# Optimization experiments

Measured on AMD Instinct MI355X. Metric: run time of the kernel, lower is better.

Reference implementation:

```python
import jax, jax.numpy as jnp
import numpy as np

# dims
B, T = 256, 64
N_AG, N_FEAT = 10, 4
X_DIM, X_PERM, X_STATIC = 44, 40, 10
HID, XEMB, NHID = 128, 32, 8
E = N_AG * (N_AG - 1)           # 90 directed edges (off-diagonal)
GEMB = NHID * E                 # 720 graph embedding per sample/step
RNN_IN = XEMB + 1 + GEMB        # 753
A_IN = X_STATIC + GEMB          # 730 (x_emb_size2==0 in GraphNN branch)
O_IN = XEMB + X_STATIC + 1 + GEMB  # 763

_off = np.ones((N_AG, N_AG)) - np.eye(N_AG)
RECV = jnp.asarray(np.where(_off)[0])  # rel_rec one-hot == gather by receiver idx
SEND = jnp.asarray(np.where(_off)[1])  # rel_send one-hot == gather by sender idx


def setup_inputs() -> dict:
    key = jax.random.key(0)
    ks = jax.random.split(key, 32)
    w = lambda k, shape: jax.random.normal(k, shape, jnp.float32) * 0.05
    return {
        'x': jax.random.normal(ks[0], (B, T + 1, X_DIM), jnp.float32),
        'x_demo': jax.random.normal(ks[1], (B, X_STATIC), jnp.float32),
        'f_treatment': jax.random.uniform(ks[2], (B, T + 1, 1), jnp.float32),
        'h0': jax.random.normal(ks[3], (B, HID), jnp.float32),
        # x2emb (Linear 4->32), x_static2emb (Linear 10->10)
        'W_x2emb': w(ks[4], (XEMB, X_DIM - X_PERM)), 'b_x2emb': w(ks[5], (XEMB,)),
        'W_stat': w(ks[6], (X_STATIC, X_STATIC)), 'b_stat': w(ks[7], (X_STATIC,)),
        # NRI-style MLP1 (node): 4->8->8 ; MLP2 (edge): 16->8->8
        'W_m1a': w(ks[8], (NHID, N_FEAT)), 'b_m1a': w(ks[9], (NHID,)),
        'W_m1b': w(ks[10], (NHID, NHID)), 'b_m1b': w(ks[11], (NHID,)),
        'W_m2a': w(ks[12], (NHID, 2 * NHID)), 'b_m2a': w(ks[13], (NHID,)),
        'W_m2b': w(ks[14], (NHID, NHID)), 'b_m2b': w(ks[15], (NHID,)),
        # treatment head: Linear(730->128)+ReLU, then Linear(128->1, no bias)
        'W_a1': w(ks[16], (HID, A_IN)), 'b_a1': w(ks[17], (HID,)),
        'W_a2': w(ks[18], (1, HID)),
        # outcome head: Linear(763->128)+ReLU, then Linear(128->1, no bias)
        'W_o1': w(ks[19], (HID, O_IN)), 'b_o1': w(ks[20], (HID,)),
        'W_o2': w(ks[21], (1, HID)),
        # GRUCell(753 -> 128)
        'W_ih': w(ks[22], (3 * HID, RNN_IN)), 'b_ih': w(ks[23], (3 * HID,)),
        'W_hh': w(ks[24], (3 * HID, HID)), 'b_hh': w(ks[25], (3 * HID,)),
    }


def reference(x, x_demo, f_treatment, h0, W_x2emb, b_x2emb, W_stat, b_stat,
              W_m1a, b_m1a, W_m1b, b_m1b, W_m2a, b_m2a, W_m2b, b_m2b,
              W_a1, b_a1, W_a2, W_o1, b_o1, W_o2, W_ih, b_ih, W_hh, b_hh):
    xt = x[:, :T]                       # (B,T,44); len_time = x.size(1)-1
    treat = f_treatment[:, :T]          # (B,T,1)
    demo = x_demo @ W_stat.T + b_stat   # (B,10) static embedding
    demoT = jnp.broadcast_to(demo[:, None], (B, T, X_STATIC))

    # --- GNN(x_permuted): mlp1 per node, node2edge gather, mlp2 per edge ---
    xa = xt[..., :X_PERM].reshape(B, T, N_AG, N_FEAT)
    h1 = jax.nn.elu(xa @ W_m1a.T + b_m1a)
    h1 = jax.nn.elu(h1 @ W_m1b.T + b_m1b)         # (B,T,N_AG,8); BN in eval = identity
    edges = jnp.concatenate([h1[:, :, RECV], h1[:, :, SEND]], axis=-1)  # (B,T,E,16)
    h2 = jax.nn.elu(edges @ W_m2a.T + b_m2a)
    h2 = jax.nn.elu(h2 @ W_m2b.T + b_m2b)         # (B,T,E,8)
    gemb = h2.reshape(B, T, GEMB)                 # (B,T,720)

    xemb = xt[..., X_PERM:] @ W_x2emb.T + b_x2emb  # (B,T,32)

    # --- treatment (a_or_ipw) head; dropout identity in eval ---
    a_in = jnp.concatenate([demoT, gemb], axis=-1)          # (B,T,730)
    a_out = jax.nn.relu(a_in @ W_a1.T + b_a1) @ W_a2.T      # (B,T,1)

    # --- outcome head ---
    o_in = jnp.concatenate([xemb, demoT, treat, gemb], axis=-1)  # (B,T,763)
    y_out = jax.nn.relu(o_in @ W_o1.T + b_o1) @ W_o2.T           # (B,T,1)

    # --- GRUCell recurrence over time ---
    rnn_in = jnp.concatenate([xemb, treat, gemb], axis=-1)  # (B,T,753)
    gi = rnn_in @ W_ih.T + b_ih                             # precompute input proj (B,T,3H)

    def step(h, g):
        gh = h @ W_hh.T + b_hh
        i_r, i_z, i_n = jnp.split(g, 3, axis=-1)
        h_r, h_z, h_n = jnp.split(gh, 3, axis=-1)
        r = jax.nn.sigmoid(i_r + h_r)
        z = jax.nn.sigmoid(i_z + h_z)
        n = jnp.tanh(i_n + r * h_n)
        h_new = (1.0 - z) * n + z * h
        return h_new, h_new

    _, hs = jax.lax.scan(step, h0, jnp.swapaxes(gi, 0, 1))
    hs = jnp.swapaxes(hs, 0, 1)                             # (B,T,128)

    return jnp.concatenate([a_out, y_out, hs], axis=-1)     # (B,T,130)
```

## Files before the change

kernel.cpp:

```cpp
#include <hip/hip_runtime.h>
#include <hip/hip_bf16.h>
#include <math.h>

#define BB     256
#define TT     64
#define BT     (BB*TT)
#define XD     44
#define XP     40
#define XS     10
#define HID    128
#define XEMB   32
#define NHID   8
#define NAG    10
#define NEDGE  90
#define GEMB   720
#define KF     768
#define NTOT   640


typedef __bf16  bf16_t;
typedef __bf16  bf16x8 __attribute__((ext_vector_type(8)));
typedef float   floatx4 __attribute__((ext_vector_type(4)));
typedef _Float16 half2_t __attribute__((ext_vector_type(2)));
typedef _Float16 half4_t __attribute__((ext_vector_type(4)));
typedef _Float16 half8_t __attribute__((ext_vector_type(8)));

__device__ __forceinline__ float rcp_fast(float x) { return __builtin_amdgcn_rcpf(x); }
__device__ __forceinline__ float sigmoid_fast(float v) { return rcp_fast(1.f + __expf(-v)); }
__device__ __forceinline__ float tanh_fast(float x) { return 1.f - 2.f * rcp_fast(1.f + __expf(2.f * x)); }
__device__ __forceinline__ float elu_fast(float v) { return v > 0.f ? v : __expf(v) - 1.f; }
__device__ __forceinline__ float fdot2f(half2_t a, half2_t b, float acc) {
  return __builtin_amdgcn_fdot2(a, b, acc, false);
}
__device__ __forceinline__ float dot8h(half8_t a, half8_t b, float acc) {
  acc = fdot2f(half2_t{a[0], a[1]}, half2_t{b[0], b[1]}, acc);
  acc = fdot2f(half2_t{a[2], a[3]}, half2_t{b[2], b[3]}, acc);
  acc = fdot2f(half2_t{a[4], a[5]}, half2_t{b[4], b[5]}, acc);
  acc = fdot2f(half2_t{a[6], a[7]}, half2_t{b[6], b[7]}, acc);
  return acc;
}
__device__ __forceinline__ void lds_barrier() {
  asm volatile("s_waitcnt lgkmcnt(0)" ::: "memory");
  __builtin_amdgcn_s_barrier();
}

__global__ __launch_bounds__(256) void prep_kernel(
    const float* __restrict__ Wa1, const float* __restrict__ ba1,
    const float* __restrict__ Wo1, const float* __restrict__ bo1,
    const float* __restrict__ Wih, const float* __restrict__ bih,
    bf16_t* __restrict__ WT, float* __restrict__ bcat) {
  int idx = blockIdx.x * 256 + threadIdx.x;
  if (idx >= NTOT * KF) return;
  int n = idx / KF, k = idx - n * KF;
  float v = 0.f;
  if (n < 128) {
    if (k >= 32 && k < 42)  v = Wa1[n * 730 + (k - 32)];
    else if (k >= 48)       v = Wa1[n * 730 + 10 + (k - 48)];
  } else if (n < 256) {
    int m = n - 128;
    if (k < 43)             v = Wo1[m * 763 + k];
    else if (k >= 48)       v = Wo1[m * 763 + 43 + (k - 48)];
  } else {
    int m = n - 256;
    if (k < 32)             v = Wih[m * 753 + k];
    else if (k == 42)       v = Wih[m * 753 + 32];
    else if (k >= 48)       v = Wih[m * 753 + 33 + (k - 48)];
  }
  WT[n * KF + k] = (bf16_t)v;
  if (k == 0) {
    bcat[n] = (n < 128) ? ba1[n] : (n < 256 ? bo1[n - 128] : bih[n - 256]);
  }
}

__global__ __launch_bounds__(64) void encoder_kernel(
    const float* __restrict__ x, const float* __restrict__ x_demo,
    const float* __restrict__ ftreat,
    const float* __restrict__ Wm1a, const float* __restrict__ bm1a,
    const float* __restrict__ Wm1b, const float* __restrict__ bm1b,
    const float* __restrict__ Wm2a, const float* __restrict__ bm2a,
    const float* __restrict__ Wm2b, const float* __restrict__ bm2b,
    const float* __restrict__ Wx2e, const float* __restrict__ bx2e,
    const float* __restrict__ Wst, const float* __restrict__ bst,
    bf16_t* __restrict__ F) {
  int blk = blockIdx.x;
  int b = blk >> 4, tc = blk & 15;
  int lane = threadIdx.x;

  __shared__ __align__(16) _Float16 h1sp[NAG * 8];
  __shared__ __align__(16) _Float16 w2aR[64];
  __shared__ __align__(16) _Float16 w2aS[64];
  __shared__ __align__(16) _Float16 w2bp[64];
  __shared__ float demoL[XS];

  if (lane < 8) {
    float4 v0 = *(const float4*)(Wm2a + lane * 16);
    float4 v1 = *(const float4*)(Wm2a + lane * 16 + 4);
    float4 v2 = *(const float4*)(Wm2a + lane * 16 + 8);
    float4 v3 = *(const float4*)(Wm2a + lane * 16 + 12);
    *(half8_t*)&w2aR[lane * 8] = half8_t{
        (_Float16)v0.x, (_Float16)v0.y, (_Float16)v0.z, (_Float16)v0.w,
        (_Float16)v1.x, (_Float16)v1.y, (_Float16)v1.z, (_Float16)v1.w};
    *(half8_t*)&w2aS[lane * 8] = half8_t{
        (_Float16)v2.x, (_Float16)v2.y, (_Float16)v2.z, (_Float16)v2.w,
        (_Float16)v3.x, (_Float16)v3.y, (_Float16)v3.z, (_Float16)v3.w};
    float4 u0 = *(const float4*)(Wm2b + lane * 8);
    float4 u1 = *(const float4*)(Wm2b + lane * 8 + 4);
    *(half8_t*)&w2bp[lane * 8] = half8_t{
        (_Float16)u0.x, (_Float16)u0.y, (_Float16)u0.z, (_Float16)u0.w,
        (_Float16)u1.x, (_Float16)u1.y, (_Float16)u1.z, (_Float16)u1.w};
  }
  if (lane < 10) {
    float s = bst[lane];
#pragma unroll
    for (int j = 0; j < 10; j++) s += x_demo[b * XS + j] * Wst[lane * 10 + j];
    demoL[lane] = s;
  }

  half4_t wA[8]; float bA[8];
  half8_t wB1[8]; float bB1[8];
  float bR[8], bG[8];
#pragma unroll
  for (int o = 0; o < 8; o++) {
    float4 v = *(const float4*)(Wm1a + o * 4);
    wA[o] = half4_t{(_Float16)v.x, (_Float16)v.y, (_Float16)v.z, (_Float16)v.w};
    bA[o] = bm1a[o];
    float4 w0 = *(const float4*)(Wm1b + o * 8);
    float4 w1 = *(const float4*)(Wm1b + o * 8 + 4);
    wB1[o] = half8_t{(_Float16)w0.x, (_Float16)w0.y, (_Float16)w0.z, (_Float16)w0.w,
                     (_Float16)w1.x, (_Float16)w1.y, (_Float16)w1.z, (_Float16)w1.w};
    bB1[o] = bm1b[o];
    bR[o] = bm2a[o];
    bG[o] = bm2b[o];
  }
  half4_t wX; float bX;
  {
    float4 v = *(const float4*)(Wx2e + (lane & 31) * 4);
    wX = half4_t{(_Float16)v.x, (_Float16)v.y, (_Float16)v.z, (_Float16)v.w};
    bX = bx2e[lane & 31];
  }
  __syncthreads();
  float demov = (lane >= 32 && lane < 42) ? demoL[lane - 32] : 0.f;

  for (int ti = 0; ti < 4; ti++) {
    int t = tc * 4 + ti;
    int tok = b * TT + t;
    const float* row = x + (size_t)(b * 65 + t) * XD;
    bf16_t* Frow = F + (size_t)tok * KF;

    if (lane < NAG) {
      float4 xa = *(const float4*)(row + lane * 4);
      half2_t x0{(_Float16)xa.x, (_Float16)xa.y};
      half2_t x1{(_Float16)xa.z, (_Float16)xa.w};
      float h1v[8];
#pragma unroll
      for (int o = 0; o < 8; o++) {
        float s = bA[o];
        s = fdot2f(x0, half2_t{wA[o][0], wA[o][1]}, s);
        s = fdot2f(x1, half2_t{wA[o][2], wA[o][3]}, s);
        h1v[o] = elu_fast(s);
      }
      half2_t e0{(_Float16)h1v[0], (_Float16)h1v[1]};
      half2_t e1{(_Float16)h1v[2], (_Float16)h1v[3]};
      half2_t e2{(_Float16)h1v[4], (_Float16)h1v[5]};
      half2_t e3{(_Float16)h1v[6], (_Float16)h1v[7]};
      half8_t hout;
#pragma unroll
      for (int o = 0; o < 8; o++) {
        float s = bB1[o];
        s = fdot2f(e0, half2_t{wB1[o][0], wB1[o][1]}, s);
        s = fdot2f(e1, half2_t{wB1[o][2], wB1[o][3]}, s);
        s = fdot2f(e2, half2_t{wB1[o][4], wB1[o][5]}, s);
        s = fdot2f(e3, half2_t{wB1[o][6], wB1[o][7]}, s);
        hout[o] = (_Float16)elu_fast(s);
      }
      *(half8_t*)&h1sp[lane * 8] = hout;
    }
    __syncthreads();

#pragma unroll
    for (int q = 0; q < 2; q++) {
      int e = lane + 64 * q;
      if (e < NEDGE) {
        int r = (e * 57) >> 9;
        int sd = e - 9 * r;
        sd += (sd >= r) ? 1 : 0;
        half8_t hr = *(const half8_t*)&h1sp[r * 8];
        half8_t hs = *(const half8_t*)&h1sp[sd * 8];
        float av[8];
#pragma unroll
        for (int o = 0; o < 8; o++) {
          half8_t wr8 = *(const half8_t*)&w2aR[o * 8];
          half8_t ws8 = *(const half8_t*)&w2aS[o * 8];
          float s = bR[o];
          s = dot8h(hr, wr8, s);
          s = dot8h(hs, ws8, s);
          av[o] = elu_fast(s);
        }
        half2_t a0{(_Float16)av[0], (_Float16)av[1]};
        half2_t a1{(_Float16)av[2], (_Float16)av[3]};
        half2_t a2{(_Float16)av[4], (_Float16)av[5]};
        half2_t a3{(_Float16)av[6], (_Float16)av[7]};
        union { bf16_t h[8]; uint4 u; } pk;
#pragma unroll
        for (int o = 0; o < 8; o++) {
          half8_t wb8 = *(const half8_t*)&w2bp[o * 8];
          float s = bG[o];
          s = fdot2f(a0, half2_t{wb8[0], wb8[1]}, s);
          s = fdot2f(a1, half2_t{wb8[2], wb8[3]}, s);
          s = fdot2f(a2, half2_t{wb8[4], wb8[5]}, s);
          s = fdot2f(a3, half2_t{wb8[6], wb8[7]}, s);
          pk.h[o] = (bf16_t)elu_fast(s);
        }
        *(uint4*)(Frow + 48 + e * 8) = pk.u;
      }
    }

    float4 xe = *(const float4*)(row + XP);
    if (lane < 32) {
      float s = bX;
      s = fdot2f(half2_t{(_Float16)xe.x, (_Float16)xe.y}, half2_t{wX[0], wX[1]}, s);
      s = fdot2f(half2_t{(_Float16)xe.z, (_Float16)xe.w}, half2_t{wX[2], wX[3]}, s);
      Frow[lane] = (bf16_t)s;
    } else if (lane < 42) {
      Frow[lane] = (bf16_t)demov;
    } else if (lane == 42) {
      Frow[42] = (bf16_t)ftreat[b * 65 + t];
    } else if (lane < 48) {
      Frow[lane] = (bf16_t)0.f;
    }
    __syncthreads();
  }
}

__global__ __launch_bounds__(256) void gemm_kernel(
    const bf16_t* __restrict__ F, const bf16_t* __restrict__ WT,
    const float* __restrict__ bcat, float* __restrict__ G) {
  __shared__ __align__(16) bf16_t As[128 * 32];
  __shared__ __align__(16) bf16_t Bs[128 * 32];

  int tid  = threadIdx.x;
  int lane = tid & 63;
  int wv   = tid >> 6;
  int wr   = wv >> 1, wc = wv & 1;
  int m0 = blockIdx.x * 128, n0 = blockIdx.y * 128;

  floatx4 acc[4][4];
#pragma unroll
  for (int i = 0; i < 4; i++)
#pragma unroll
    for (int j = 0; j < 4; j++) acc[i][j] = floatx4{0.f, 0.f, 0.f, 0.f};

  int c0 = tid, c1 = tid + 256;
  int r0 = c0 >> 2, p0 = c0 & 3;
  int r1 = c1 >> 2, p1 = c1 & 3;
  int qr = lane >> 4;
  int lr = lane & 15;

  for (int k0 = 0; k0 < KF; k0 += 32) {
    uint4 a0 = *(const uint4*)(F  + (size_t)(m0 + r0) * KF + k0 + p0 * 8);
    uint4 a1 = *(const uint4*)(F  + (size_t)(m0 + r1) * KF + k0 + p1 * 8);
    uint4 b0 = *(const uint4*)(WT + (size_t)(n0 + r0) * KF + k0 + p0 * 8);
    uint4 b1 = *(const uint4*)(WT + (size_t)(n0 + r1) * KF + k0 + p1 * 8);
    __syncthreads();
    ((uint4*)As)[c0] = a0; ((uint4*)As)[c1] = a1;
    ((uint4*)Bs)[c0] = b0; ((uint4*)Bs)[c1] = b1;
    __syncthreads();

    bf16x8 af[4], bf[4];
#pragma unroll
    for (int i = 0; i < 4; i++) {
      af[i] = *(const bf16x8*)(As + (wr * 64 + i * 16 + lr) * 32 + qr * 8);
      bf[i] = *(const bf16x8*)(Bs + (wc * 64 + i * 16 + lr) * 32 + qr * 8);
    }
#pragma unroll
    for (int i = 0; i < 4; i++)
#pragma unroll
      for (int j = 0; j < 4; j++)
        acc[i][j] = __builtin_amdgcn_mfma_f32_16x16x32_bf16(af[i], bf[j], acc[i][j], 0, 0, 0);
  }

#pragma unroll
  for (int i = 0; i < 4; i++) {
#pragma unroll
    for (int j = 0; j < 4; j++) {
      int col = n0 + wc * 64 + j * 16 + lr;
      float bv = bcat[col];
#pragma unroll
      for (int r = 0; r < 4; r++) {
        int row = m0 + wr * 64 + i * 16 + qr * 4 + r;
        G[(size_t)row * NTOT + col] = acc[i][j][r] + bv;
      }
    }
  }
}

__global__ __launch_bounds__(256) void head_kernel(
    const float* __restrict__ G, const float* __restrict__ Wa2,
    const float* __restrict__ Wo2, float* __restrict__ out) {
  int wid  = (blockIdx.x * 256 + threadIdx.x) >> 6;
  int lane = threadIdx.x & 63;
  const float* g = G + (size_t)wid * NTOT;
  float sa = fmaxf(g[lane], 0.f) * Wa2[lane] + fmaxf(g[lane + 64], 0.f) * Wa2[lane + 64];
  float sy = fmaxf(g[128 + lane], 0.f) * Wo2[lane] + fmaxf(g[192 + lane], 0.f) * Wo2[lane + 64];
#pragma unroll
  for (int off = 32; off > 0; off >>= 1) {
    sa += __shfl_down(sa, off, 64);
    sy += __shfl_down(sy, off, 64);
  }
  if (lane == 0) {
    out[(size_t)wid * 130 + 0] = sa;
    out[(size_t)wid * 130 + 1] = sy;
  }
}

__global__ __launch_bounds__(128, 1) void gru_kernel(
    const float* __restrict__ G, const float* __restrict__ h0,
    const float* __restrict__ Whh, const float* __restrict__ bhh,
    float* __restrict__ out) {
  int b = blockIdx.x;
  int tid = threadIdx.x;
  int lane = tid & 63;

  __shared__ unsigned int h2[2][HID / 2];

  const float* gbase = G + (size_t)b * TT * NTOT;

  half2_t wr[64], wz[64], wn[64];
#pragma unroll
  for (int l = 0; l < 64; l++) {
    float2 a = *(const float2*)(Whh + (size_t)tid * HID + 2 * l);
    wr[l] = half2_t{(_Float16)a.x, (_Float16)a.y};
  }
#pragma unroll
  for (int l = 0; l < 64; l++) {
    float2 a = *(const float2*)(Whh + (size_t)(HID + tid) * HID + 2 * l);
    wz[l] = half2_t{(_Float16)a.x, (_Float16)a.y};
  }
#pragma unroll
  for (int l = 0; l < 64; l++) {
    float2 a = *(const float2*)(Whh + (size_t)(2 * HID + tid) * HID + 2 * l);
    wn[l] = half2_t{(_Float16)a.x, (_Float16)a.y};
  }
  float br = bhh[tid], bz = bhh[HID + tid], bn = bhh[2 * HID + tid];

  float hprev = h0[(size_t)b * HID + tid];
  ((_Float16*)h2[0])[tid] = (_Float16)hprev;
  float ir = gbase[256 + tid], iz = gbase[384 + tid], inn = gbase[512 + tid];
  __syncthreads();

  for (int t = 0; t < TT; t++) {
    unsigned int hl = h2[t & 1][lane];
    float nir = 0.f, niz = 0.f, ninn = 0.f;
    if (t + 1 < TT) {
      const float* gn = gbase + (size_t)(t + 1) * NTOT;
      nir  = gn[256 + tid];
      niz  = gn[384 + tid];
      ninn = gn[512 + tid];
    }
    float sr0 = 0.f, sr1 = 0.f, sz0 = 0.f, sz1 = 0.f, sn0 = 0.f, sn1 = 0.f;
#pragma unroll
    for (int l = 0; l < 64; l += 2) {
      int p0 = __builtin_amdgcn_readlane((int)hl, l);
      int p1 = __builtin_amdgcn_readlane((int)hl, l + 1);
      half2_t q0 = __builtin_bit_cast(half2_t, p0);
      half2_t q1 = __builtin_bit_cast(half2_t, p1);
      sr0 = __builtin_amdgcn_fdot2(wr[l],     q0, sr0, false);
      sr1 = __builtin_amdgcn_fdot2(wr[l + 1], q1, sr1, false);
      sz0 = __builtin_amdgcn_fdot2(wz[l],     q0, sz0, false);
      sz1 = __builtin_amdgcn_fdot2(wz[l + 1], q1, sz1, false);
      sn0 = __builtin_amdgcn_fdot2(wn[l],     q0, sn0, false);
      sn1 = __builtin_amdgcn_fdot2(wn[l + 1], q1, sn1, false);
    }
    float r  = sigmoid_fast(ir + sr0 + sr1 + br);
    float z  = sigmoid_fast(iz + sz0 + sz1 + bz);
    float nn = tanh_fast(inn + r * (sn0 + sn1 + bn));
    float hn = (1.f - z) * nn + z * hprev;
    hprev = hn;
    ((_Float16*)h2[(t + 1) & 1])[tid] = (_Float16)hn;
    lds_barrier();
    out[(size_t)(b * TT + t) * 130 + 2 + tid] = hn;
    ir = nir; iz = niz; inn = ninn;
  }
}

extern "C" void kernel_launch(void* const* d_in, const int* in_sizes, int n_in,
                              void* d_out, int out_size, void* d_ws, size_t ws_size,
                              hipStream_t stream) {
  const float* x      = (const float*)d_in[0];
  const float* x_demo = (const float*)d_in[1];
  const float* ftr    = (const float*)d_in[2];
  const float* h0     = (const float*)d_in[3];
  const float* Wx2e   = (const float*)d_in[4];
  const float* bx2e   = (const float*)d_in[5];
  const float* Wst    = (const float*)d_in[6];
  const float* bst    = (const float*)d_in[7];
  const float* Wm1a   = (const float*)d_in[8];
  const float* bm1a   = (const float*)d_in[9];
  const float* Wm1b   = (const float*)d_in[10];
  const float* bm1b   = (const float*)d_in[11];
  const float* Wm2a   = (const float*)d_in[12];
  const float* bm2a   = (const float*)d_in[13];
  const float* Wm2b   = (const float*)d_in[14];
  const float* bm2b   = (const float*)d_in[15];
  const float* Wa1    = (const float*)d_in[16];
  const float* ba1    = (const float*)d_in[17];
  const float* Wa2    = (const float*)d_in[18];
  const float* Wo1    = (const float*)d_in[19];
  const float* bo1    = (const float*)d_in[20];
  const float* Wo2    = (const float*)d_in[21];
  const float* Wih    = (const float*)d_in[22];
  const float* bih    = (const float*)d_in[23];
  const float* Whh    = (const float*)d_in[24];
  const float* bhh    = (const float*)d_in[25];
  float* out = (float*)d_out;

  char* ws = (char*)d_ws;
  bf16_t* F   = (bf16_t*)(ws);
  bf16_t* WT  = (bf16_t*)(ws + 25165824);
  float*  bc  = (float*)(ws + 25165824 + 983040);
  float*  G   = (float*)(ws + 25165824 + 983040 + 2560);

  prep_kernel<<<dim3((NTOT * KF + 255) / 256), dim3(256), 0, stream>>>(
      Wa1, ba1, Wo1, bo1, Wih, bih, WT, bc);
  encoder_kernel<<<dim3(BB * 16), dim3(64), 0, stream>>>(
      x, x_demo, ftr, Wm1a, bm1a, Wm1b, bm1b, Wm2a, bm2a, Wm2b, bm2b,
      Wx2e, bx2e, Wst, bst, F);
  gemm_kernel<<<dim3(BT / 128, NTOT / 128), dim3(256), 0, stream>>>(F, WT, bc, G);
  head_kernel<<<dim3(BT / 4), dim3(256), 0, stream>>>(G, Wa2, Wo2, out);
  gru_kernel<<<dim3(BB), dim3(128), 0, stream>>>(G, h0, Whh, bhh, out);
}
```

Baseline: 228.5 us.

## Batch GRU recurrence over 16 samples per block using bf16 MFMA

The GRU kernel changes from one block per sample, which did dot products with fdot2 and readlane broadcasts of fp16 hidden state, to one block per 16 samples. Each step's h·W_hh product now runs on 16x16x32 bf16 MFMA instructions, with the weight fragments held in registers and the hidden state transposed through double-buffered LDS. The aim is to cut the per-step latency of the serial 64-step recurrence. The trade-offs are that only 16 blocks occupy the GPU and the hidden state is rounded to bf16 instead of fp16, which may reduce accuracy.

```diff
diff --git a/kernel.cpp b/kernel.cpp
--- a/kernel.cpp
+++ b/kernel.cpp
@@ -19,6 +19,7 @@
 
 
 typedef __bf16  bf16_t;
+typedef __bf16  bf16x4 __attribute__((ext_vector_type(4)));
 typedef __bf16  bf16x8 __attribute__((ext_vector_type(8)));
 typedef float   floatx4 __attribute__((ext_vector_type(4)));
 typedef _Float16 half2_t __attribute__((ext_vector_type(2)));
@@ -313,73 +314,117 @@
   }
 }
 
-__global__ __launch_bounds__(128, 1) void gru_kernel(
+__global__ __launch_bounds__(256, 1) void gru_kernel(
     const float* __restrict__ G, const float* __restrict__ h0,
     const float* __restrict__ Whh, const float* __restrict__ bhh,
     float* __restrict__ out) {
-  int b = blockIdx.x;
-  int tid = threadIdx.x;
+  int tid  = threadIdx.x;
+  int w    = tid >> 6;
   int lane = tid & 63;
-
-  __shared__ unsigned int h2[2][HID / 2];
-
-  const float* gbase = G + (size_t)b * TT * NTOT;
-
-  half2_t wr[64], wz[64], wn[64];
-#pragma unroll
-  for (int l = 0; l < 64; l++) {
-    float2 a = *(const float2*)(Whh + (size_t)tid * HID + 2 * l);
-    wr[l] = half2_t{(_Float16)a.x, (_Float16)a.y};
-  }
-#pragma unroll
-  for (int l = 0; l < 64; l++) {
-    float2 a = *(const float2*)(Whh + (size_t)(HID + tid) * HID + 2 * l);
-    wz[l] = half2_t{(_Float16)a.x, (_Float16)a.y};
-  }
-#pragma unroll
-  for (int l = 0; l < 64; l++) {
-    float2 a = *(const float2*)(Whh + (size_t)(2 * HID + tid) * HID + 2 * l);
-    wn[l] = half2_t{(_Float16)a.x, (_Float16)a.y};
-  }
-  float br = bhh[tid], bz = bhh[HID + tid], bn = bhh[2 * HID + tid];
-
-  float hprev = h0[(size_t)b * HID + tid];
-  ((_Float16*)h2[0])[tid] = (_Float16)hprev;
-  float ir = gbase[256 + tid], iz = gbase[384 + tid], inn = gbase[512 + tid];
+  int l15  = lane & 15;
+  int quad = lane >> 4;
+  int b0   = blockIdx.x * 16;
+  int s    = b0 + l15;
+
+  __shared__ __align__(16) bf16_t hT[2][16 * 136];
+
+  bf16x8 afrag[6][4];
+#pragma unroll
+  for (int g = 0; g < 3; g++) {
+#pragma unroll
+    for (int tp = 0; tp < 2; tp++) {
+      const float* wrow = Whh + (size_t)(g * 128 + w * 32 + tp * 16 + l15) * HID + quad * 8;
+#pragma unroll
+      for (int ks = 0; ks < 4; ks++) {
+        float4 a = *(const float4*)(wrow + ks * 32);
+        float4 b = *(const float4*)(wrow + ks * 32 + 4);
+        afrag[g * 2 + tp][ks] = bf16x8{
+            (bf16_t)a.x, (bf16_t)a.y, (bf16_t)a.z, (bf16_t)a.w,
+            (bf16_t)b.x, (bf16_t)b.y, (bf16_t)b.z, (bf16_t)b.w};
+      }
+    }
+  }
+  int jb0 = w * 32 + quad * 4;
+  int jb1 = jb0 + 16;
+  floatx4 biasv[6];
+#pragma unroll
+  for (int g = 0; g < 3; g++) {
+    biasv[g * 2 + 0] = *(const floatx4*)(bhh + g * 128 + jb0);
+    biasv[g * 2 + 1] = *(const floatx4*)(bhh + g * 128 + jb1);
+  }
+  floatx4 hprev[2];
+  hprev[0] = *(const floatx4*)(h0 + (size_t)s * HID + jb0);
+  hprev[1] = *(const floatx4*)(h0 + (size_t)s * HID + jb1);
+
+  {
+    int sq = tid >> 4, u = (tid & 15) * 8;
+    const float* hr = h0 + (size_t)(b0 + sq) * HID + u;
+    float4 a = *(const float4*)hr;
+    float4 b = *(const float4*)(hr + 4);
+    *(bf16x8*)&hT[0][sq * 136 + u] = bf16x8{
+        (bf16_t)a.x, (bf16_t)a.y, (bf16_t)a.z, (bf16_t)a.w,
+        (bf16_t)b.x, (bf16_t)b.y, (bf16_t)b.z, (bf16_t)b.w};
+  }
+  const float* grow = G + (size_t)s * TT * NTOT;
+  floatx4 gi[6];
+#pragma unroll
+  for (int g = 0; g < 3; g++) {
+    gi[g * 2 + 0] = *(const floatx4*)(grow + 256 + g * 128 + jb0);
+    gi[g * 2 + 1] = *(const floatx4*)(grow + 256 + g * 128 + jb1);
+  }
   __syncthreads();
 
+  float* obase = out + (size_t)s * TT * 130 + 2;
+
   for (int t = 0; t < TT; t++) {
-    unsigned int hl = h2[t & 1][lane];
-    float nir = 0.f, niz = 0.f, ninn = 0.f;
+    const bf16_t* hb = &hT[t & 1][l15 * 136 + quad * 8];
+    bf16x8 bfrag[4];
+#pragma unroll
+    for (int ks = 0; ks < 4; ks++) bfrag[ks] = *(const bf16x8*)(hb + ks * 32);
+
+    floatx4 ngi[6];
     if (t + 1 < TT) {
-      const float* gn = gbase + (size_t)(t + 1) * NTOT;
-      nir  = gn[256 + tid];
-      niz  = gn[384 + tid];
-      ninn = gn[512 + tid];
-    }
-    float sr0 = 0.f, sr1 = 0.f, sz0 = 0.f, sz1 = 0.f, sn0 = 0.f, sn1 = 0.f;
-#pragma unroll
-    for (int l = 0; l < 64; l += 2) {
-      int p0 = __builtin_amdgcn_readlane((int)hl, l);
-      int p1 = __builtin_amdgcn_readlane((int)hl, l + 1);
-      half2_t q0 = __builtin_bit_cast(half2_t, p0);
-      half2_t q1 = __builtin_bit_cast(half2_t, p1);
-      sr0 = __builtin_amdgcn_fdot2(wr[l],     q0, sr0, false);
-      sr1 = __builtin_amdgcn_fdot2(wr[l + 1], q1, sr1, false);
-      sz0 = __builtin_amdgcn_fdot2(wz[l],     q0, sz0, false);
-      sz1 = __builtin_amdgcn_fdot2(wz[l + 1], q1, sz1, false);
-      sn0 = __builtin_amdgcn_fdot2(wn[l],     q0, sn0, false);
-      sn1 = __builtin_amdgcn_fdot2(wn[l + 1], q1, sn1, false);
-    }
-    float r  = sigmoid_fast(ir + sr0 + sr1 + br);
-    float z  = sigmoid_fast(iz + sz0 + sz1 + bz);
-    float nn = tanh_fast(inn + r * (sn0 + sn1 + bn));
-    float hn = (1.f - z) * nn + z * hprev;
-    hprev = hn;
-    ((_Float16*)h2[(t + 1) & 1])[tid] = (_Float16)hn;
+      const float* gn = grow + NTOT;
+#pragma unroll
+      for (int g = 0; g < 3; g++) {
+        ngi[g * 2 + 0] = *(const floatx4*)(gn + 256 + g * 128 + jb0);
+        ngi[g * 2 + 1] = *(const floatx4*)(gn + 256 + g * 128 + jb1);
+      }
+    }
+
+    floatx4 acc[6];
+#pragma unroll
+    for (int i = 0; i < 6; i++) acc[i] = biasv[i];
+#pragma unroll
+    for (int ks = 0; ks < 4; ks++)
+#pragma unroll
+      for (int i = 0; i < 6; i++)
+        acc[i] = __builtin_amdgcn_mfma_f32_16x16x32_bf16(afrag[i][ks], bfrag[ks], acc[i], 0, 0, 0);
+
+#pragma unroll
+    for (int tp = 0; tp < 2; tp++) {
+      int jb = tp ? jb1 : jb0;
+      floatx4 hn;
+#pragma unroll
+      for (int r = 0; r < 4; r++) {
+        float rr = sigmoid_fast(gi[0 + tp][r] + acc[0 + tp][r]);
+        float zz = sigmoid_fast(gi[2 + tp][r] + acc[2 + tp][r]);
+        float nn = tanh_fast(gi[4 + tp][r] + rr * acc[4 + tp][r]);
+        hn[r] = (1.f - zz) * nn + zz * hprev[tp][r];
+      }
+      hprev[tp] = hn;
+      *(bf16x4*)&hT[(t + 1) & 1][l15 * 136 + jb] = bf16x4{
+          (bf16_t)hn[0], (bf16_t)hn[1], (bf16_t)hn[2], (bf16_t)hn[3]};
+      float* ob = obase + jb;
+      *(float2*)ob       = float2{hn[0], hn[1]};
+      *(float2*)(ob + 2) = float2{hn[2], hn[3]};
+    }
+
     lds_barrier();
-    out[(size_t)(b * TT + t) * 130 + 2 + tid] = hn;
-    ir = nir; iz = niz; inn = ninn;
+#pragma unroll
+    for (int i = 0; i < 6; i++) gi[i] = ngi[i];
+    grow  += NTOT;
+    obase += 130;
   }
 }
 
@@ -427,5 +472,5 @@
       Wx2e, bx2e, Wst, bst, F);
   gemm_kernel<<<dim3(BT / 128, NTOT / 128), dim3(256), 0, stream>>>(F, WT, bc, G);
   head_kernel<<<dim3(BT / 4), dim3(256), 0, stream>>>(G, Wa2, Wo2, out);
-  gru_kernel<<<dim3(BB), dim3(128), 0, stream>>>(G, h0, Whh, bhh, out);
-}
+  gru_kernel<<<dim3(BB / 16), dim3(256), 0, stream>>>(G, h0, Whh, bhh, out);
+}
```

Result: slower. 263.3 us (+15.3%).
